# Optimization experiments

Measured on AMD Instinct MI355X. Metric: run time of the kernel, lower is better.

The kernel has to match this reference:

```python
import jax, jax.numpy as jnp
import numpy as np

N_HEADS = 32
N_KV_HEADS = 8
HEAD_DIM = 128
GROUP = N_HEADS // N_KV_HEADS  # 4
MAX_SEQ_LEN = 4096
DIM = 3072
NEG_BIG = 1.0e9


def setup_inputs() -> dict:
    key = jax.random.key(0)
    ks = jax.random.split(key, 8)
    B, T = 1, 2048
    return {
        "x": jax.random.normal(ks[0], (B, T, DIM), dtype=jnp.float32),
        "freqs_cos": jax.random.uniform(ks[1], (T, HEAD_DIM // 2), dtype=jnp.float32),
        "freqs_sin": jax.random.uniform(ks[2], (T, HEAD_DIM // 2), dtype=jnp.float32),
        "input_pos": jnp.arange(T, dtype=jnp.int32),
        "wq": jax.random.normal(ks[3], (N_HEADS * HEAD_DIM, DIM), dtype=jnp.float32) * 0.02,
        "wk": jax.random.normal(ks[4], (N_KV_HEADS * HEAD_DIM, DIM), dtype=jnp.float32) * 0.02,
        "wv": jax.random.normal(ks[5], (N_KV_HEADS * HEAD_DIM, DIM), dtype=jnp.float32) * 0.02,
        "wo": jax.random.normal(ks[6], (DIM, N_HEADS * HEAD_DIM), dtype=jnp.float32) * 0.02,
        "k_cache": jnp.zeros((1, N_KV_HEADS, MAX_SEQ_LEN, HEAD_DIM), dtype=jnp.float32),
        "v_cache": jnp.zeros((1, N_KV_HEADS, MAX_SEQ_LEN, HEAD_DIM), dtype=jnp.float32),
    }


def _rotate_half(x):
    half = x.shape[-1] // 2
    return jnp.concatenate([-x[..., half:], x[..., :half]], axis=-1)


def _apply_rope(q, k, freqs_cos, freqs_sin):
    # freqs: [T, D/2] -> [1, T, 1, D] (tiled x2, matching torch repeat on last dim)
    fc = jnp.concatenate([freqs_cos, freqs_cos], axis=-1)[None, :, None, :]
    fs = jnp.concatenate([freqs_sin, freqs_sin], axis=-1)[None, :, None, :]
    qf = q.astype(jnp.float32)
    kf = k.astype(jnp.float32)
    q_out = qf * fc + _rotate_half(qf) * fs
    k_out = kf * fc + _rotate_half(kf) * fs
    return q_out.astype(q.dtype), k_out.astype(k.dtype)


def reference(x, freqs_cos, freqs_sin, input_pos, wq, wk, wv, wo, k_cache, v_cache):
    B, T, _ = x.shape
    # QKV projections
    q = (x @ wq.T).reshape(B, T, N_HEADS, HEAD_DIM)
    k = (x @ wk.T).reshape(B, T, N_KV_HEADS, HEAD_DIM)
    v = (x @ wv.T).reshape(B, T, N_KV_HEADS, HEAD_DIM)
    # split-half RoPE (computed in fp32)
    q, k = _apply_rope(q, k, freqs_cos, freqs_sin)
    # StaticKVCache.update: scatter [B,H,T,D] into [1,H,S,D] cache at input_pos (dim 2)
    kc = k_cache.at[:, :, input_pos].set(k.transpose(0, 2, 1, 3))
    vc = v_cache.at[:, :, input_pos].set(v.transpose(0, 2, 1, 3))
    # MetalSDPA: additive causal mask over full cache length
    S = kc.shape[2]
    k_pos = jnp.arange(S)
    valid = jnp.clip(input_pos[:, None] - k_pos[None, :] + 1, 0, 1)  # [T, S]
    mask = (valid.astype(q.dtype) - 1.0) * NEG_BIG
    # GQA attention: group q heads per kv head
    qg = q.transpose(0, 2, 1, 3).reshape(B, N_KV_HEADS, GROUP, T, HEAD_DIM)
    scale = 1.0 / jnp.sqrt(jnp.asarray(HEAD_DIM, dtype=q.dtype))
    scores = jnp.einsum('bhgtd,bhsd->bhgts', qg, kc) * scale + mask  # [B,Hk,G,T,S]
    attn = jax.nn.softmax(scores, axis=-1)
    y = jnp.einsum('bhgts,bhsd->bhgtd', attn, vc)
    y = y.reshape(B, N_HEADS, T, HEAD_DIM).transpose(0, 2, 1, 3).reshape(B, T, N_HEADS * HEAD_DIM)
    return y @ wo.T
```

## Files before the change

### kernel.cpp

```cpp
#include <hip/hip_runtime.h>

typedef __attribute__((ext_vector_type(8))) short bf16x8;
typedef __attribute__((ext_vector_type(4))) float f32x4;

#define T_SEQ   2048
#define DIM     3072
#define NQH     32
#define NKVH    8
#define HD      128
#define QDIM    4096
#define KVDIM   1024
#define QKVDIM  6144

#define AS1 __attribute__((address_space(1)))
#define AS3 __attribute__((address_space(3)))

static __device__ __forceinline__ unsigned short f2bf(float f) {
  unsigned u = __float_as_uint(f);
  u += 0x7FFFu + ((u >> 16) & 1u);
  return (unsigned short)(u >> 16);
}
static __device__ __forceinline__ float bf2f(unsigned short h) {
  return __uint_as_float(((unsigned)h) << 16);
}

static __device__ __forceinline__ void gload_lds16(const unsigned short* g, unsigned short* l) {
  __builtin_amdgcn_global_load_lds((AS1 void*)(g), (AS3 void*)(l), 16, 0, 0);
}

__global__ void cvt_f32_bf16(const float* __restrict__ src, unsigned short* __restrict__ dst, int n4) {
  int i = blockIdx.x * blockDim.x + threadIdx.x;
  if (i >= n4) return;
  float4 v = reinterpret_cast<const float4*>(src)[i];
  ushort4 o;
  o.x = f2bf(v.x); o.y = f2bf(v.y); o.z = f2bf(v.z); o.w = f2bf(v.w);
  reinterpret_cast<ushort4*>(dst)[i] = o;
}

template<int OUTBF>
__global__ __launch_bounds__(256) void gemm_bt(
    const unsigned short* __restrict__ A, const unsigned short* __restrict__ B,
    float* __restrict__ Cf, unsigned short* __restrict__ Cb,
    int M, int N, int K) {
  __shared__ unsigned short la[128 * 64];
  __shared__ unsigned short lb[128 * 64];
  const int nbx = N >> 7;
  const int q8 = gridDim.x >> 3;
  int bid = blockIdx.x;
  bid = (bid & 7) * q8 + (bid >> 3);
  const int bx = bid % nbx, by = bid / nbx;
  const int tid = threadIdx.x;
  const int ln = tid & 63;
  const int wave = tid >> 6;
  const int lr = ln & 15, lg = ln >> 4;
  const int wr = wave >> 1, wc = wave & 1;
  const int rowA0 = by << 7, rowB0 = bx << 7;

  f32x4 acc[4][4] = {};

  const int ktn = K >> 6;
  for (int kt = 0; kt < ktn; kt++) {
    __syncthreads();
#pragma unroll
    for (int it = 0; it < 4; it++) {
      int ci = it * 256 + tid;
      int r = ci >> 3, cpos = ci & 7;
      int c = cpos ^ (r & 7);
      const unsigned short* gA = A + (size_t)(rowA0 + r) * K + kt * 64 + c * 8;
      const unsigned short* gB = B + (size_t)(rowB0 + r) * K + kt * 64 + c * 8;
      gload_lds16(gA, &la[ci * 8]);
      gload_lds16(gB, &lb[ci * 8]);
    }
    __syncthreads();
#pragma unroll
    for (int kk = 0; kk < 2; kk++) {
      bf16x8 af[4], bfr[4];
#pragma unroll
      for (int mi = 0; mi < 4; mi++) {
        int r = wr * 64 + mi * 16 + lr;
        int p = (kk * 4 + lg) ^ (r & 7);
        af[mi] = *reinterpret_cast<const bf16x8*>(&la[r * 64 + p * 8]);
      }
#pragma unroll
      for (int ni = 0; ni < 4; ni++) {
        int r = wc * 64 + ni * 16 + lr;
        int p = (kk * 4 + lg) ^ (r & 7);
        bfr[ni] = *reinterpret_cast<const bf16x8*>(&lb[r * 64 + p * 8]);
      }
#pragma unroll
      for (int mi = 0; mi < 4; mi++)
#pragma unroll
        for (int ni = 0; ni < 4; ni++)
          acc[mi][ni] = __builtin_amdgcn_mfma_f32_16x16x32_bf16(af[mi], bfr[ni], acc[mi][ni], 0, 0, 0);
    }
  }
#pragma unroll
  for (int mi = 0; mi < 4; mi++)
#pragma unroll
    for (int ni = 0; ni < 4; ni++)
#pragma unroll
      for (int j = 0; j < 4; j++) {
        int r = rowA0 + wr * 64 + mi * 16 + lg * 4 + j;
        int cc = rowB0 + wc * 64 + ni * 16 + lr;
        if (OUTBF) Cb[(size_t)r * N + cc] = f2bf(acc[mi][ni][j]);
        else       Cf[(size_t)r * N + cc] = acc[mi][ni][j];
      }
}

__global__ void rope_repack(const unsigned short* __restrict__ qkv,
                            const float* __restrict__ fc, const float* __restrict__ fs,
                            unsigned short* __restrict__ qo, unsigned short* __restrict__ ko) {
  int idx = blockIdx.x * blockDim.x + threadIdx.x;
  int d = idx & 63;
  int hh = (idx >> 6) % 40;
  int t = idx / 2560;
  const unsigned short* src = qkv + (size_t)t * QKVDIM + hh * 128;
  float x0 = bf2f(src[d]);
  float x1 = bf2f(src[d + 64]);
  float c = fc[t * 64 + d], s = fs[t * 64 + d];
  float o0 = x0 * c - x1 * s;
  float o1 = x1 * c + x0 * s;
  if (hh < 32) {
    unsigned short* dst = qo + (size_t)t * QDIM + hh * 128;
    dst[d] = f2bf(o0); dst[d + 64] = f2bf(o1);
  } else {
    unsigned short* dst = ko + (size_t)t * KVDIM + (hh - 32) * 128;
    dst[d] = f2bf(o0); dst[d + 64] = f2bf(o1);
  }
}

__global__ void vtrans(const unsigned short* __restrict__ qkv, unsigned short* __restrict__ vt) {
  __shared__ unsigned short tile[64][68];
  int tb = blockIdx.x * 64, cb = blockIdx.y * 64;
  int tid = threadIdx.x;
#pragma unroll
  for (int i = 0; i < 16; i++) {
    int e = i * 256 + tid;
    int tl = e >> 6, cl = e & 63;
    tile[tl][cl] = qkv[(size_t)(tb + tl) * QKVDIM + 5120 + cb + cl];
  }
  __syncthreads();
#pragma unroll
  for (int i = 0; i < 16; i++) {
    int e = i * 256 + tid;
    int cl = e >> 6, tl = e & 63;
    vt[(size_t)(cb + cl) * T_SEQ + tb + tl] = tile[tl][cl];
  }
}

__global__ __launch_bounds__(256) void attn_fwd(
    const unsigned short* __restrict__ q, const unsigned short* __restrict__ k,
    const unsigned short* __restrict__ vt, unsigned short* __restrict__ y) {
  __shared__ unsigned short k_lds[2][32 * 128];
  __shared__ unsigned short v_lds[2][128 * 32];
  __shared__ unsigned short p_lds[4][16 * 40];
  __shared__ float a_lds[4][16];
  const int tid = threadIdx.x;
  const int ln = tid & 63;
  const int wave = tid >> 6;
  const int lr = ln & 15, lg = ln >> 4;

  const int kh = blockIdx.x & 7;
  const int i = blockIdx.x >> 3;
  const int qh = i & 3;
  const int qt = 31 - (i >> 2);
  const int h = kh * 4 + qh;

  const int qr0 = qt * 64 + wave * 16;
  const int qrow = qr0 + lr;
  const float SL2E = 0.08838834764831845f * 1.44269504088896f;
  const float NEGINF = -__builtin_inff();

  bf16x8 qf[4];
  const unsigned short* qb = q + (size_t)qrow * QDIM + h * HD + lg * 8;
#pragma unroll
  for (int dc = 0; dc < 4; dc++) qf[dc] = *reinterpret_cast<const bf16x8*>(qb + dc * 32);

  f32x4 acc[8] = {};
  float m = NEGINF, lsum = 0.f;

  const int krow0 = tid >> 4,      kcol0 = tid & 15;
  const int krow1 = 16 + krow0;
  const int vrow0 = tid >> 2,      vcol0 = tid & 3;
  const int vrow1 = 64 + vrow0;

  const int ntiles = (qt * 64 + 95) >> 5;

  {
    bf16x8 kr0 = *reinterpret_cast<const bf16x8*>(k + (size_t)krow0 * KVDIM + kh * HD + kcol0 * 8);
    bf16x8 kr1 = *reinterpret_cast<const bf16x8*>(k + (size_t)krow1 * KVDIM + kh * HD + kcol0 * 8);
    bf16x8 vr0 = *reinterpret_cast<const bf16x8*>(vt + (size_t)(kh * HD + vrow0) * T_SEQ + vcol0 * 8);
    bf16x8 vr1 = *reinterpret_cast<const bf16x8*>(vt + (size_t)(kh * HD + vrow1) * T_SEQ + vcol0 * 8);
    *reinterpret_cast<bf16x8*>(&k_lds[0][krow0 * 128 + (kcol0 ^ (krow0 & 7)) * 8]) = kr0;
    *reinterpret_cast<bf16x8*>(&k_lds[0][krow1 * 128 + (kcol0 ^ (krow1 & 7)) * 8]) = kr1;
    *reinterpret_cast<bf16x8*>(&v_lds[0][vrow0 * 32 + (vcol0 ^ ((vrow0 >> 1) & 3)) * 8]) = vr0;
    *reinterpret_cast<bf16x8*>(&v_lds[0][vrow1 * 32 + (vcol0 ^ ((vrow1 >> 1) & 3)) * 8]) = vr1;
  }
  __syncthreads();

  for (int st = 0; st < ntiles; st++) {
    const int sb = st * 32;
    const int cur = st & 1;
    const bool more = (st + 1 < ntiles);

    bf16x8 kr0, kr1, vr0, vr1;
    if (more) {
      const int sb1 = sb + 32;
      kr0 = *reinterpret_cast<const bf16x8*>(k + (size_t)(sb1 + krow0) * KVDIM + kh * HD + kcol0 * 8);
      kr1 = *reinterpret_cast<const bf16x8*>(k + (size_t)(sb1 + krow1) * KVDIM + kh * HD + kcol0 * 8);
      vr0 = *reinterpret_cast<const bf16x8*>(vt + (size_t)(kh * HD + vrow0) * T_SEQ + sb1 + vcol0 * 8);
      vr1 = *reinterpret_cast<const bf16x8*>(vt + (size_t)(kh * HD + vrow1) * T_SEQ + sb1 + vcol0 * 8);
    }

    if (sb <= qr0 + 15) {
      f32x4 s0t = {0.f, 0.f, 0.f, 0.f}, s1t = {0.f, 0.f, 0.f, 0.f};
      __builtin_amdgcn_s_setprio(1);
#pragma unroll
      for (int dc = 0; dc < 4; dc++) {
        int c = lg + dc * 4;
        int p = c ^ (lr & 7);
        bf16x8 a0 = *reinterpret_cast<const bf16x8*>(&k_lds[cur][lr * 128 + p * 8]);
        bf16x8 a1 = *reinterpret_cast<const bf16x8*>(&k_lds[cur][(lr + 16) * 128 + p * 8]);
        s0t = __builtin_amdgcn_mfma_f32_16x16x32_bf16(a0, qf[dc], s0t, 0, 0, 0);
        s1t = __builtin_amdgcn_mfma_f32_16x16x32_bf16(a1, qf[dc], s1t, 0, 0, 0);
      }
      __builtin_amdgcn_s_setprio(0);

      float vv[8];
      if (sb + 31 <= qr0) {
#pragma unroll
        for (int jj = 0; jj < 4; jj++) { vv[jj] = s0t[jj]; vv[jj + 4] = s1t[jj]; }
      } else {
        const int base0 = sb + lg * 4;
#pragma unroll
        for (int jj = 0; jj < 4; jj++) {
          vv[jj]     = (base0 + jj      <= qrow) ? s0t[jj] : NEGINF;
          vv[jj + 4] = (base0 + jj + 16 <= qrow) ? s1t[jj] : NEGINF;
        }
      }

      float mx = fmaxf(fmaxf(fmaxf(vv[0], vv[1]), fmaxf(vv[2], vv[3])),
                       fmaxf(fmaxf(vv[4], vv[5]), fmaxf(vv[6], vv[7])));
      mx = fmaxf(mx, __shfl_xor(mx, 16));
      mx = fmaxf(mx, __shfl_xor(mx, 32));

      const bool doresc = __any(mx > m + 60.0f);
      const float mn = doresc ? fmaxf(m, mx) : m;

      float p[8], ps = 0.f;
#pragma unroll
      for (int ii = 0; ii < 8; ii++) { p[ii] = exp2f((vv[ii] - mn) * SL2E); ps += p[ii]; }
      ps += __shfl_xor(ps, 16);
      ps += __shfl_xor(ps, 32);

      ushort4 pw0, pw1;
      pw0.x = f2bf(p[0]); pw0.y = f2bf(p[1]); pw0.z = f2bf(p[2]); pw0.w = f2bf(p[3]);
      pw1.x = f2bf(p[4]); pw1.y = f2bf(p[5]); pw1.z = f2bf(p[6]); pw1.w = f2bf(p[7]);
      *reinterpret_cast<ushort4*>(&p_lds[wave][lr * 40 + lg * 4])      = pw0;
      *reinterpret_cast<ushort4*>(&p_lds[wave][lr * 40 + 16 + lg * 4]) = pw1;

      if (doresc) {
        const float alpha = exp2f((m - mn) * SL2E);
        lsum = lsum * alpha + ps;
        m = mn;
        a_lds[wave][lr] = alpha;
        asm volatile("s_waitcnt lgkmcnt(0)" ::: "memory");
        float4 a4 = *reinterpret_cast<const float4*>(&a_lds[wave][lg * 4]);
#pragma unroll
        for (int dc2 = 0; dc2 < 8; dc2++) {
          acc[dc2][0] *= a4.x; acc[dc2][1] *= a4.y;
          acc[dc2][2] *= a4.z; acc[dc2][3] *= a4.w;
        }
      } else {
        lsum += ps;
        asm volatile("s_waitcnt lgkmcnt(0)" ::: "memory");
      }

      bf16x8 pa = *reinterpret_cast<const bf16x8*>(&p_lds[wave][lr * 40 + lg * 8]);
      __builtin_amdgcn_s_setprio(1);
#pragma unroll
      for (int dc2 = 0; dc2 < 8; dc2++) {
        int d = dc2 * 16 + lr;
        int p2 = lg ^ ((d >> 1) & 3);
        bf16x8 bv = *reinterpret_cast<const bf16x8*>(&v_lds[cur][d * 32 + p2 * 8]);
        acc[dc2] = __builtin_amdgcn_mfma_f32_16x16x32_bf16(pa, bv, acc[dc2], 0, 0, 0);
      }
      __builtin_amdgcn_s_setprio(0);
    }

    if (more) {
      const int nxt = cur ^ 1;
      *reinterpret_cast<bf16x8*>(&k_lds[nxt][krow0 * 128 + (kcol0 ^ (krow0 & 7)) * 8]) = kr0;
      *reinterpret_cast<bf16x8*>(&k_lds[nxt][krow1 * 128 + (kcol0 ^ (krow1 & 7)) * 8]) = kr1;
      *reinterpret_cast<bf16x8*>(&v_lds[nxt][vrow0 * 32 + (vcol0 ^ ((vrow0 >> 1) & 3)) * 8]) = vr0;
      *reinterpret_cast<bf16x8*>(&v_lds[nxt][vrow1 * 32 + (vcol0 ^ ((vrow1 >> 1) & 3)) * 8]) = vr1;
      __syncthreads();
    }
  }

  a_lds[wave][lr] = 1.0f / lsum;
  asm volatile("s_waitcnt lgkmcnt(0)" ::: "memory");
  float4 l4 = *reinterpret_cast<const float4*>(&a_lds[wave][lg * 4]);
  float li[4] = {l4.x, l4.y, l4.z, l4.w};
#pragma unroll
  for (int jj = 0; jj < 4; jj++) {
    int r = qr0 + lg * 4 + jj;
#pragma unroll
    for (int dc2 = 0; dc2 < 8; dc2++)
      y[(size_t)r * QDIM + h * HD + dc2 * 16 + lr] = f2bf(acc[dc2][jj] * li[jj]);
  }
}

extern "C" void kernel_launch(void* const* d_in, const int* in_sizes, int n_in,
                              void* d_out, int out_size, void* d_ws, size_t ws_size,
                              hipStream_t stream) {
  (void)in_sizes; (void)n_in; (void)out_size; (void)ws_size;
  const float* x    = (const float*)d_in[0];
  const float* fcos = (const float*)d_in[1];
  const float* fsin = (const float*)d_in[2];
  const float* wq   = (const float*)d_in[4];
  const float* wk   = (const float*)d_in[5];
  const float* wv   = (const float*)d_in[6];
  const float* wo   = (const float*)d_in[7];
  float* out = (float*)d_out;
  char* ws = (char*)d_ws;

  unsigned short* x_bf    = (unsigned short*)(ws);
  unsigned short* wqkv_bf = (unsigned short*)(ws + 12582912);
  unsigned short* qkv_bf  = (unsigned short*)(ws + 50331648);
  unsigned short* q_bf    = (unsigned short*)(ws);
  unsigned short* k_bf    = (unsigned short*)(ws + 16777216);
  unsigned short* vt_bf   = (unsigned short*)(ws + 20971520);
  unsigned short* y_bf    = (unsigned short*)(ws + 25165824);
  unsigned short* wo_bf   = (unsigned short*)(ws + 50331648);

  cvt_f32_bf16<<<6144,  256, 0, stream>>>(x,  x_bf,               2048 * 3072 / 4);
  cvt_f32_bf16<<<12288, 256, 0, stream>>>(wq, wqkv_bf,            4096 * 3072 / 4);
  cvt_f32_bf16<<<3072,  256, 0, stream>>>(wk, wqkv_bf + 4096*3072, 1024 * 3072 / 4);
  cvt_f32_bf16<<<3072,  256, 0, stream>>>(wv, wqkv_bf + 5120*3072, 1024 * 3072 / 4);
  gemm_bt<1><<<768, 256, 0, stream>>>(x_bf, wqkv_bf, nullptr, qkv_bf, 2048, 6144, 3072);

  rope_repack<<<20480, 256, 0, stream>>>(qkv_bf, fcos, fsin, q_bf, k_bf);
  vtrans<<<dim3(32, 16), 256, 0, stream>>>(qkv_bf, vt_bf);

  cvt_f32_bf16<<<12288, 256, 0, stream>>>(wo, wo_bf, 3072 * 4096 / 4);
  attn_fwd<<<1024, 256, 0, stream>>>(q_bf, k_bf, vt_bf, y_bf);
  gemm_bt<0><<<384, 256, 0, stream>>>(y_bf, wo_bf, out, nullptr, 2048, 3072, 4096);
}
```

Baseline: 329.6 us.

## Pair mirrored causal query tiles per block to balance work and reuse K/V tiles

Each attention block now handles two query tiles, pr and 31-pr, so every block does about the same amount of causal work. The K/V tiles loaded into LDS are shared by both tiles. The grid is halved to 512 blocks. P is also converted to bf16 with the packed v_cvt_pk_bf16_f32 instruction. In exchange, register pressure roughly doubles because there are two accumulator sets, which may lower occupancy, and there are fewer blocks in flight.

```diff
diff --git a/kernel.cpp b/kernel.cpp
--- a/kernel.cpp
+++ b/kernel.cpp
@@ -22,6 +22,11 @@
 }
 static __device__ __forceinline__ float bf2f(unsigned short h) {
   return __uint_as_float(((unsigned)h) << 16);
+}
+static __device__ __forceinline__ unsigned pkbf(float lo, float hi) {
+  unsigned r;
+  asm("v_cvt_pk_bf16_f32 %0, %1, %2" : "=v"(r) : "v"(lo), "v"(hi));
+  return r;
 }
 
 static __device__ __forceinline__ void gload_lds16(const unsigned short* g, unsigned short* l) {
@@ -163,28 +168,112 @@
   const int kh = blockIdx.x & 7;
   const int i = blockIdx.x >> 3;
   const int qh = i & 3;
-  const int qt = 31 - (i >> 2);
+  const int pr = i >> 2;
+  const int qta = pr, qtb = 31 - pr;
   const int h = kh * 4 + qh;
 
-  const int qr0 = qt * 64 + wave * 16;
-  const int qrow = qr0 + lr;
+  const int qra0 = qta * 64 + wave * 16, qrowa = qra0 + lr;
+  const int qrb0 = qtb * 64 + wave * 16, qrowb = qrb0 + lr;
   const float SL2E = 0.08838834764831845f * 1.44269504088896f;
   const float NEGINF = -__builtin_inff();
 
-  bf16x8 qf[4];
-  const unsigned short* qb = q + (size_t)qrow * QDIM + h * HD + lg * 8;
-#pragma unroll
-  for (int dc = 0; dc < 4; dc++) qf[dc] = *reinterpret_cast<const bf16x8*>(qb + dc * 32);
-
-  f32x4 acc[8] = {};
-  float m = NEGINF, lsum = 0.f;
-
-  const int krow0 = tid >> 4,      kcol0 = tid & 15;
+  bf16x8 qfa[4], qfb[4];
+  {
+    const unsigned short* qba = q + (size_t)qrowa * QDIM + h * HD + lg * 8;
+    const unsigned short* qbb = q + (size_t)qrowb * QDIM + h * HD + lg * 8;
+#pragma unroll
+    for (int dc = 0; dc < 4; dc++) {
+      qfa[dc] = *reinterpret_cast<const bf16x8*>(qba + dc * 32);
+      qfb[dc] = *reinterpret_cast<const bf16x8*>(qbb + dc * 32);
+    }
+  }
+
+  f32x4 acca[8] = {}, accb[8] = {};
+  float ma = NEGINF, la = 0.f, mb = NEGINF, lb = 0.f;
+
+  const int krow0 = tid >> 4,  kcol0 = tid & 15;
   const int krow1 = 16 + krow0;
-  const int vrow0 = tid >> 2,      vcol0 = tid & 3;
+  const int vrow0 = tid >> 2,  vcol0 = tid & 3;
   const int vrow1 = 64 + vrow0;
 
-  const int ntiles = (qt * 64 + 95) >> 5;
+  auto tile_compute = [&](int sb, int cur, const bf16x8 (&qf)[4], f32x4 (&acc)[8],
+                          float& m, float& lsum, int qr0, int qrow) {
+    f32x4 s0t = {0.f, 0.f, 0.f, 0.f}, s1t = {0.f, 0.f, 0.f, 0.f};
+    __builtin_amdgcn_s_setprio(1);
+#pragma unroll
+    for (int dc = 0; dc < 4; dc++) {
+      int c = lg + dc * 4;
+      int p = c ^ (lr & 7);
+      bf16x8 a0 = *reinterpret_cast<const bf16x8*>(&k_lds[cur][lr * 128 + p * 8]);
+      bf16x8 a1 = *reinterpret_cast<const bf16x8*>(&k_lds[cur][(lr + 16) * 128 + p * 8]);
+      s0t = __builtin_amdgcn_mfma_f32_16x16x32_bf16(a0, qf[dc], s0t, 0, 0, 0);
+      s1t = __builtin_amdgcn_mfma_f32_16x16x32_bf16(a1, qf[dc], s1t, 0, 0, 0);
+    }
+    __builtin_amdgcn_s_setprio(0);
+
+    float vv[8];
+    if (sb + 31 <= qr0) {
+#pragma unroll
+      for (int jj = 0; jj < 4; jj++) { vv[jj] = s0t[jj]; vv[jj + 4] = s1t[jj]; }
+    } else {
+      const int base0 = sb + lg * 4;
+#pragma unroll
+      for (int jj = 0; jj < 4; jj++) {
+        vv[jj]     = (base0 + jj      <= qrow) ? s0t[jj] : NEGINF;
+        vv[jj + 4] = (base0 + jj + 16 <= qrow) ? s1t[jj] : NEGINF;
+      }
+    }
+
+    float mx = fmaxf(fmaxf(fmaxf(vv[0], vv[1]), fmaxf(vv[2], vv[3])),
+                     fmaxf(fmaxf(vv[4], vv[5]), fmaxf(vv[6], vv[7])));
+    mx = fmaxf(mx, __shfl_xor(mx, 16));
+    mx = fmaxf(mx, __shfl_xor(mx, 32));
+
+    const bool doresc = __any(mx > m + 60.0f);
+    const float mn = doresc ? fmaxf(m, mx) : m;
+
+    float p[8], ps = 0.f;
+#pragma unroll
+    for (int ii = 0; ii < 8; ii++) { p[ii] = exp2f((vv[ii] - mn) * SL2E); ps += p[ii]; }
+    ps += __shfl_xor(ps, 16);
+    ps += __shfl_xor(ps, 32);
+
+    uint2 w0, w1;
+    w0.x = pkbf(p[0], p[1]); w0.y = pkbf(p[2], p[3]);
+    w1.x = pkbf(p[4], p[5]); w1.y = pkbf(p[6], p[7]);
+    *reinterpret_cast<uint2*>(&p_lds[wave][lr * 40 + lg * 4])      = w0;
+    *reinterpret_cast<uint2*>(&p_lds[wave][lr * 40 + 16 + lg * 4]) = w1;
+
+    if (doresc) {
+      const float alpha = exp2f((m - mn) * SL2E);
+      lsum = lsum * alpha + ps;
+      m = mn;
+      a_lds[wave][lr] = alpha;
+      asm volatile("s_waitcnt lgkmcnt(0)" ::: "memory");
+      float4 a4 = *reinterpret_cast<const float4*>(&a_lds[wave][lg * 4]);
+#pragma unroll
+      for (int dc2 = 0; dc2 < 8; dc2++) {
+        acc[dc2][0] *= a4.x; acc[dc2][1] *= a4.y;
+        acc[dc2][2] *= a4.z; acc[dc2][3] *= a4.w;
+      }
+    } else {
+      lsum += ps;
+      asm volatile("s_waitcnt lgkmcnt(0)" ::: "memory");
+    }
+
+    bf16x8 pa = *reinterpret_cast<const bf16x8*>(&p_lds[wave][lr * 40 + lg * 8]);
+    __builtin_amdgcn_s_setprio(1);
+#pragma unroll
+    for (int dc2 = 0; dc2 < 8; dc2++) {
+      int d = dc2 * 16 + lr;
+      int p2 = lg ^ ((d >> 1) & 3);
+      bf16x8 bv = *reinterpret_cast<const bf16x8*>(&v_lds[cur][d * 32 + p2 * 8]);
+      acc[dc2] = __builtin_amdgcn_mfma_f32_16x16x32_bf16(pa, bv, acc[dc2], 0, 0, 0);
+    }
+    __builtin_amdgcn_s_setprio(0);
+  };
+
+  const int ntiles = (qtb * 64 + 95) >> 5;
 
   {
     bf16x8 kr0 = *reinterpret_cast<const bf16x8*>(k + (size_t)krow0 * KVDIM + kh * HD + kcol0 * 8);
@@ -212,81 +301,8 @@
       vr1 = *reinterpret_cast<const bf16x8*>(vt + (size_t)(kh * HD + vrow1) * T_SEQ + sb1 + vcol0 * 8);
     }
 
-    if (sb <= qr0 + 15) {
-      f32x4 s0t = {0.f, 0.f, 0.f, 0.f}, s1t = {0.f, 0.f, 0.f, 0.f};
-      __builtin_amdgcn_s_setprio(1);
-#pragma unroll
-      for (int dc = 0; dc < 4; dc++) {
-        int c = lg + dc * 4;
-        int p = c ^ (lr & 7);
-        bf16x8 a0 = *reinterpret_cast<const bf16x8*>(&k_lds[cur][lr * 128 + p * 8]);
-        bf16x8 a1 = *reinterpret_cast<const bf16x8*>(&k_lds[cur][(lr + 16) * 128 + p * 8]);
-        s0t = __builtin_amdgcn_mfma_f32_16x16x32_bf16(a0, qf[dc], s0t, 0, 0, 0);
-        s1t = __builtin_amdgcn_mfma_f32_16x16x32_bf16(a1, qf[dc], s1t, 0, 0, 0);
-      }
-      __builtin_amdgcn_s_setprio(0);
-
-      float vv[8];
-      if (sb + 31 <= qr0) {
-#pragma unroll
-        for (int jj = 0; jj < 4; jj++) { vv[jj] = s0t[jj]; vv[jj + 4] = s1t[jj]; }
-      } else {
-        const int base0 = sb + lg * 4;
-#pragma unroll
-        for (int jj = 0; jj < 4; jj++) {
-          vv[jj]     = (base0 + jj      <= qrow) ? s0t[jj] : NEGINF;
-          vv[jj + 4] = (base0 + jj + 16 <= qrow) ? s1t[jj] : NEGINF;
-        }
-      }
-
-      float mx = fmaxf(fmaxf(fmaxf(vv[0], vv[1]), fmaxf(vv[2], vv[3])),
-                       fmaxf(fmaxf(vv[4], vv[5]), fmaxf(vv[6], vv[7])));
-      mx = fmaxf(mx, __shfl_xor(mx, 16));
-      mx = fmaxf(mx, __shfl_xor(mx, 32));
-
-      const bool doresc = __any(mx > m + 60.0f);
-      const float mn = doresc ? fmaxf(m, mx) : m;
-
-      float p[8], ps = 0.f;
-#pragma unroll
-      for (int ii = 0; ii < 8; ii++) { p[ii] = exp2f((vv[ii] - mn) * SL2E); ps += p[ii]; }
-      ps += __shfl_xor(ps, 16);
-      ps += __shfl_xor(ps, 32);
-
-      ushort4 pw0, pw1;
-      pw0.x = f2bf(p[0]); pw0.y = f2bf(p[1]); pw0.z = f2bf(p[2]); pw0.w = f2bf(p[3]);
-      pw1.x = f2bf(p[4]); pw1.y = f2bf(p[5]); pw1.z = f2bf(p[6]); pw1.w = f2bf(p[7]);
-      *reinterpret_cast<ushort4*>(&p_lds[wave][lr * 40 + lg * 4])      = pw0;
-      *reinterpret_cast<ushort4*>(&p_lds[wave][lr * 40 + 16 + lg * 4]) = pw1;
-
-      if (doresc) {
-        const float alpha = exp2f((m - mn) * SL2E);
-        lsum = lsum * alpha + ps;
-        m = mn;
-        a_lds[wave][lr] = alpha;
-        asm volatile("s_waitcnt lgkmcnt(0)" ::: "memory");
-        float4 a4 = *reinterpret_cast<const float4*>(&a_lds[wave][lg * 4]);
-#pragma unroll
-        for (int dc2 = 0; dc2 < 8; dc2++) {
-          acc[dc2][0] *= a4.x; acc[dc2][1] *= a4.y;
-          acc[dc2][2] *= a4.z; acc[dc2][3] *= a4.w;
-        }
-      } else {
-        lsum += ps;
-        asm volatile("s_waitcnt lgkmcnt(0)" ::: "memory");
-      }
-
-      bf16x8 pa = *reinterpret_cast<const bf16x8*>(&p_lds[wave][lr * 40 + lg * 8]);
-      __builtin_amdgcn_s_setprio(1);
-#pragma unroll
-      for (int dc2 = 0; dc2 < 8; dc2++) {
-        int d = dc2 * 16 + lr;
-        int p2 = lg ^ ((d >> 1) & 3);
-        bf16x8 bv = *reinterpret_cast<const bf16x8*>(&v_lds[cur][d * 32 + p2 * 8]);
-        acc[dc2] = __builtin_amdgcn_mfma_f32_16x16x32_bf16(pa, bv, acc[dc2], 0, 0, 0);
-      }
-      __builtin_amdgcn_s_setprio(0);
-    }
+    if (sb <= qrb0 + 15) tile_compute(sb, cur, qfb, accb, mb, lb, qrb0, qrowb);
+    if (sb <= qra0 + 15) tile_compute(sb, cur, qfa, acca, ma, la, qra0, qrowa);
 
     if (more) {
       const int nxt = cur ^ 1;
@@ -298,16 +314,31 @@
     }
   }
 
-  a_lds[wave][lr] = 1.0f / lsum;
+  a_lds[wave][lr] = 1.0f / lb;
   asm volatile("s_waitcnt lgkmcnt(0)" ::: "memory");
   float4 l4 = *reinterpret_cast<const float4*>(&a_lds[wave][lg * 4]);
-  float li[4] = {l4.x, l4.y, l4.z, l4.w};
-#pragma unroll
-  for (int jj = 0; jj < 4; jj++) {
-    int r = qr0 + lg * 4 + jj;
-#pragma unroll
-    for (int dc2 = 0; dc2 < 8; dc2++)
-      y[(size_t)r * QDIM + h * HD + dc2 * 16 + lr] = f2bf(acc[dc2][jj] * li[jj]);
+  {
+    float li[4] = {l4.x, l4.y, l4.z, l4.w};
+#pragma unroll
+    for (int jj = 0; jj < 4; jj++) {
+      int r = qrb0 + lg * 4 + jj;
+#pragma unroll
+      for (int dc2 = 0; dc2 < 8; dc2++)
+        y[(size_t)r * QDIM + h * HD + dc2 * 16 + lr] = f2bf(accb[dc2][jj] * li[jj]);
+    }
+  }
+  a_lds[wave][lr] = 1.0f / la;
+  asm volatile("s_waitcnt lgkmcnt(0)" ::: "memory");
+  l4 = *reinterpret_cast<const float4*>(&a_lds[wave][lg * 4]);
+  {
+    float li[4] = {l4.x, l4.y, l4.z, l4.w};
+#pragma unroll
+    for (int jj = 0; jj < 4; jj++) {
+      int r = qra0 + lg * 4 + jj;
+#pragma unroll
+      for (int dc2 = 0; dc2 < 8; dc2++)
+        y[(size_t)r * QDIM + h * HD + dc2 * 16 + lr] = f2bf(acca[dc2][jj] * li[jj]);
+    }
   }
 }
 
@@ -344,6 +375,6 @@
   vtrans<<<dim3(32, 16), 256, 0, stream>>>(qkv_bf, vt_bf);
 
   cvt_f32_bf16<<<12288, 256, 0, stream>>>(wo, wo_bf, 3072 * 4096 / 4);
-  attn_fwd<<<1024, 256, 0, stream>>>(q_bf, k_bf, vt_bf, y_bf);
+  attn_fwd<<<512, 256, 0, stream>>>(q_bf, k_bf, vt_bf, y_bf);
   gemm_bt<0><<<384, 256, 0, stream>>>(y_bf, wo_bf, out, nullptr, 2048, 3072, 4096);
 }
```

Result: no change. 326.5 us (-0.9%).
